# Kernel tuning notes

Measured on AMD Instinct MI355X. Metric: run time of the kernel, lower is better.

Reference implementation:

```python
import jax, jax.numpy as jnp
import numpy as np
from jax import lax

CW = 8       # current_window
PW = 8       # pretrain_window
HEADS = 8
LOG100 = float(np.log(100.0))


def setup_inputs() -> dict:
    key = jax.random.key(0)
    ks = jax.random.split(key, 8)
    B, H, W, C = 8, 126, 126, 256
    f32 = jnp.float32
    return {
        "x": jax.random.normal(ks[0], (B, H, W, C), f32),
        "w_qkv": jax.random.normal(ks[1], (C, 3 * C), f32) * 0.02,      # 1x1 conv, no bias
        "w_dw": jax.random.normal(ks[2], (3, 3, 1, 3 * C), f32) * 0.1,  # depthwise 3x3, HWIO
        "ln_gamma": jnp.ones((3 * C,), f32),
        "ln_beta": jnp.zeros((3 * C,), f32),
        "q_bias": jnp.zeros((C,), f32),
        "v_bias": jnp.zeros((C,), f32),
        "scale": jnp.full((HEADS, 1, 1), np.log(10.0), f32),
        "cpb_w0": jax.random.normal(ks[3], (2, 512), f32) * 0.02,
        "cpb_b0": jnp.zeros((512,), f32),
        "cpb_w1": jax.random.normal(ks[4], (512, HEADS), f32) * 0.02,   # no bias, sigmoid
        "w_proj": jax.random.normal(ks[5], (C, C), f32) * 0.02,
    }


def _l2n(t):
    # tf.math.l2_normalize with epsilon=1.55e-5
    return t * lax.rsqrt(jnp.maximum(jnp.sum(t * t, axis=-1, keepdims=True), 1.55e-5))


def _cpb_bias(cpb_w0, cpb_b0, cpb_w1, cw, L, heads):
    # log-spaced continuous relative position table (static)
    rel = np.arange(1 - cw, cw, dtype=np.float32)
    rel = np.stack(np.meshgrid(rel, rel, indexing='ij'), axis=-1)  # [2cw-1, 2cw-1, 2]
    rel = rel * (8.0 / (PW - 1.0))
    rel = np.sign(rel) * np.log1p(np.abs(rel)) / np.log(8.0)
    ri = np.arange(cw)
    ri = np.stack(np.meshgrid(ri, ri, indexing='ij'), axis=0).reshape(2, -1)
    ri = ri[:, :, None] - ri[:, None, :] + (cw - 1)
    relidx = (ri[0] * (2 * cw - 1) + ri[1]).reshape(-1)  # [L*L]
    h = jax.nn.relu(jnp.asarray(rel.reshape(-1, 2)) @ cpb_w0 + cpb_b0)
    bias = jax.nn.sigmoid(h @ cpb_w1) * 16.0             # [(2cw-1)^2, heads]
    bias = bias[jnp.asarray(relidx)].reshape(L, L, heads)
    return bias.transpose(2, 0, 1)                        # [heads, L, L]


def reference(x, w_qkv, w_dw, ln_gamma, ln_beta, q_bias, v_bias, scale,
              cpb_w0, cpb_b0, cpb_w1, w_proj):
    B, H, W, C = x.shape
    cw, heads = CW, HEADS
    hd = C // heads
    L = cw * cw

    # qkv 1x1 conv + depthwise 3x3 + layernorm (ConvNorm)
    qkv = jnp.einsum('bhwc,cd->bhwd', x, w_qkv)           # [B,H,W,3C]
    qkv = lax.conv_general_dilated(qkv, w_dw, (1, 1), 'SAME',
                                   dimension_numbers=('NHWC', 'HWIO', 'NHWC'),
                                   feature_group_count=3 * C)
    mu = jnp.mean(qkv, axis=-1, keepdims=True)
    var = jnp.mean(jnp.square(qkv - mu), axis=-1, keepdims=True)
    qkv = (qkv - mu) * lax.rsqrt(var + 1e-5) * ln_gamma + ln_beta
    qkv = qkv + jnp.concatenate([q_bias, jnp.zeros_like(q_bias), v_bias])

    # pad to multiple of window, grid-partition (MaxViT-style strided grid)
    pad_h, pad_w = (-H) % cw, (-W) % cw
    hb, wb = pad_h // 2, pad_w // 2
    qkv = jnp.pad(qkv, ((0, 0), (hb, pad_h - hb), (wb, pad_w - wb), (0, 0)))
    Hp, Wp = H + pad_h, W + pad_w
    Hb, Wb = Hp // cw, Wp // cw
    nw = Hb * Wb
    qkv = qkv.reshape(B, cw, Hb, cw, Wb, 3, heads, hd)
    qkv = qkv.transpose(0, 2, 4, 6, 1, 3, 5, 7).reshape(B * nw, heads, L, 3, hd)
    q, k, v = qkv[..., 0, :], qkv[..., 1, :], qkv[..., 2, :]

    # cosine attention with learned per-head log-scale (clamped at log 100)
    q, k = _l2n(q), _l2n(k)
    ls = jnp.exp(jnp.minimum(scale, LOG100))              # [heads,1,1]
    attn = jnp.einsum('nhqd,nhkd->nhqk', q * ls, k)

    attn = attn + _cpb_bias(cpb_w0, cpb_b0, cpb_w1, cw, L, heads)[None]

    if pad_h + pad_w > 0:
        m = jnp.pad(jnp.ones((1, H, W, 1), attn.dtype),
                    ((0, 0), (hb, pad_h - hb), (wb, pad_w - wb), (0, 0)))
        m = m.reshape(1, cw, Hb, cw, Wb, 1).transpose(0, 2, 4, 1, 3, 5).reshape(nw, L)
        mbias = -100.0 * (m == 0).astype(attn.dtype)       # [nw, L] over keys
        attn = attn.reshape(B, nw, heads, L, L) + mbias[None, :, None, None, :]
        attn = attn.reshape(B * nw, heads, L, L)

    attn = jax.nn.softmax(attn, axis=-1)
    out = jnp.einsum('nhqk,nhkd->nhqd', attn, v)           # [B*nw, heads, L, hd]

    # reverse grid partition + crop + projection
    out = out.reshape(B, Hb, Wb, heads, cw, cw, hd)
    out = out.transpose(0, 4, 1, 5, 2, 3, 6).reshape(B, Hp, Wp, C)
    out = out[:, hb:hb + H, wb:wb + W]
    return jnp.einsum('bhwc,cd->bhwd', out, w_proj)
```

## Files before the change

### kernel.cpp

```cpp
#include <hip/hip_runtime.h>

typedef unsigned short ushort;
typedef __bf16 bf16x8 __attribute__((ext_vector_type(8)));
typedef float f32x4 __attribute__((ext_vector_type(4)));
typedef float f4 __attribute__((ext_vector_type(4)));
typedef unsigned short us8 __attribute__((ext_vector_type(8)));
typedef unsigned short us4 __attribute__((ext_vector_type(4)));
typedef unsigned u32x4v __attribute__((ext_vector_type(4)));

#define NPIX 127008
#define HDIM 126
#define WDIM 126

__device__ __forceinline__ float bf2f(ushort u) {
  unsigned v = ((unsigned)u) << 16;
  return __builtin_bit_cast(float, v);
}
__device__ __forceinline__ ushort f2bf(float f) {
  unsigned x = __builtin_bit_cast(unsigned, f);
  x += 0x7fffu + ((x >> 16) & 1u);
  return (ushort)(x >> 16);
}

__global__ void k_cvt_x(const float* __restrict__ x, ushort* __restrict__ xb, int n8) {
  const int stride = gridDim.x * blockDim.x;
  for (int i = blockIdx.x * blockDim.x + threadIdx.x; i < n8; i += stride) {
    const f4 a = *(const f4*)&x[(size_t)i * 8];
    const f4 b = *(const f4*)&x[(size_t)i * 8 + 4];
    us8 o;
#pragma unroll
    for (int j = 0; j < 4; ++j) { o[j] = f2bf(a[j]); o[4 + j] = f2bf(b[j]); }
    *(us8*)&xb[(size_t)i * 8] = o;
  }
}

__global__ void k_cvt_wT(const float* __restrict__ in, ushort* __restrict__ out, int N, int K) {
  const int t = blockIdx.x * 256 + threadIdx.x;
  const int n = t / K, k = t - n * K;
  out[t] = f2bf(in[(size_t)k * N + n]);
}

__device__ __forceinline__ float frel(int i) {
  const float v = (float)(i - 7) * (8.0f / 7.0f);
  const float a = log1pf(fabsf(v)) * 0.4808983469629878f;
  return v < 0.f ? -a : a;
}

__global__ __launch_bounds__(256) void k_cpb1(const float* __restrict__ w0,
    const float* __restrict__ b0, const float* __restrict__ w1, float* __restrict__ tmp) {
  const int p = blockIdx.x * 4 + (threadIdx.x >> 6);
  const int lane = threadIdx.x & 63;
  if (p >= 225) return;
  const float r0 = frel(p / 15), r1 = frel(p % 15);
  float hv[8];
#pragma unroll
  for (int jj = 0; jj < 8; ++jj) {
    const int j = lane * 8 + jj;
    hv[jj] = fmaxf(0.f, r0 * w0[j] + r1 * w0[512 + j] + b0[j]);
  }
  for (int h = 0; h < 8; ++h) {
    float part = 0.f;
#pragma unroll
    for (int jj = 0; jj < 8; ++jj) part += hv[jj] * w1[(lane * 8 + jj) * 8 + h];
    for (int o = 32; o; o >>= 1) part += __shfl_xor(part, o);
    if (lane == 0) tmp[p * 8 + h] = 16.f / (1.f + __expf(-part));
  }
}

__global__ void k_cpb2(const float* __restrict__ tmp, float* __restrict__ biasV) {
  const int t = blockIdx.x * 256 + threadIdx.x;
  const int h = t >> 12, rest = t & 4095;
  const int ki = rest >> 10, g = (rest >> 8) & 3, q = (rest >> 2) & 63, r = rest & 3;
  const int key = ki * 16 + g * 4 + r;
  const int d0 = (q >> 3) - (key >> 3) + 7, d1 = (q & 7) - (key & 7) + 7;
  biasV[t] = tmp[(d0 * 15 + d1) * 8 + h];
}

#define GLL(g, l) __builtin_amdgcn_global_load_lds( \
    (const __attribute__((address_space(1))) void*)(g), \
    (__attribute__((address_space(3))) void*)(l), 16, 0, 0)

template <int OUTF, int NX>
__global__ __launch_bounds__(256) void k_gemm(const ushort* __restrict__ A,
                                              const ushort* __restrict__ Bt,
                                              void* __restrict__ Cv, int M, int N) {
  constexpr int K = 256;
  __shared__ ushort lsA[128 * 32];
  __shared__ ushort lsB[128 * 32];
  const int tid = threadIdx.x;
  const int wid = tid >> 6, lane = tid & 63;

  const int nwg = gridDim.x;
  const int q8 = nwg >> 3, r8 = nwg & 7;
  const int xcd = blockIdx.x & 7, pos = blockIdx.x >> 3;
  const int lin = (xcd < r8) ? xcd * (q8 + 1) + pos
                             : r8 * (q8 + 1) + (xcd - r8) * q8 + pos;
  const int m0 = (lin / NX) * 128, n0 = (lin % NX) * 128;

  f32x4 acc[4][4];
#pragma unroll
  for (int i = 0; i < 4; ++i)
#pragma unroll
    for (int j = 0; j < 4; ++j) acc[i][j] = 0.f;

  const int srow = tid >> 2, sk = (tid & 3) * 8;
  const int aw = (wid >> 1) * 64, bw = (wid & 1) * 64;
  const int fr = lane & 15, kg = (lane >> 4) * 8;
  char* lA = (char*)lsA + wid * 1024;
  char* lB = (char*)lsB + wid * 1024;

  int ra0 = m0 + srow;      if (ra0 >= M) ra0 = M - 1;
  int ra1 = m0 + srow + 64; if (ra1 >= M) ra1 = M - 1;
  const int rb0 = n0 + srow, rb1 = n0 + srow + 64;

  for (int kt = 0; kt < K; kt += 32) {
    __syncthreads();
    GLL(A + (size_t)ra0 * K + kt + sk, lA);
    GLL(A + (size_t)ra1 * K + kt + sk, lA + 4096);
    GLL(Bt + (size_t)rb0 * K + kt + sk, lB);
    GLL(Bt + (size_t)rb1 * K + kt + sk, lB + 4096);
    __syncthreads();
    bf16x8 af[4], bb[4];
#pragma unroll
    for (int i = 0; i < 4; ++i)
      af[i] = *(const bf16x8*)&lsA[(aw + i * 16 + fr) * 32 + kg];
#pragma unroll
    for (int j = 0; j < 4; ++j)
      bb[j] = *(const bf16x8*)&lsB[(bw + j * 16 + fr) * 32 + kg];
#pragma unroll
    for (int i = 0; i < 4; ++i)
#pragma unroll
      for (int j = 0; j < 4; ++j)
        acc[i][j] = __builtin_amdgcn_mfma_f32_16x16x32_bf16(af[i], bb[j], acc[i][j], 0, 0, 0);
  }

  const int r4 = (lane >> 4) * 4, cc = lane & 15;
#pragma unroll
  for (int i = 0; i < 4; ++i) {
#pragma unroll
    for (int j = 0; j < 4; ++j) {
      const int gc = n0 + bw + j * 16 + cc;
#pragma unroll
      for (int r = 0; r < 4; ++r) {
        const int gr = m0 + aw + i * 16 + r4 + r;
        if (gr < M) {
          if constexpr (OUTF == 0)
            ((ushort*)Cv)[(size_t)gr * N + gc] = f2bf(acc[i][j][r]);
          else
            ((float*)Cv)[(size_t)gr * N + gc] = acc[i][j][r];
        }
      }
    }
  }
}

__global__ __launch_bounds__(192) void k_convln(const ushort* __restrict__ pre,
    const float* __restrict__ wdw,
    const float* __restrict__ gamma, const float* __restrict__ beta,
    const float* __restrict__ qb, const float* __restrict__ vb,
    const float* __restrict__ scale, ushort* __restrict__ qkvw) {
  __shared__ __align__(16) float red[2][3][4];
  const int nwg = gridDim.x;
  const int q8 = nwg >> 3, r8 = nwg & 7;
  const int xcd = blockIdx.x & 7, pos = blockIdx.x >> 3;
  const int lin = (xcd < r8) ? xcd * (q8 + 1) + pos
                             : r8 * (q8 + 1) + (xcd - r8) * q8 + pos;
  const int rowid = lin % 1008;
  const int seg = lin / 1008;
  const int b = rowid / HDIM, h = rowid - b * HDIM;
  const int chunk = threadIdx.x;
  const int wid = chunk >> 6, lane = chunk & 63;
  const int c0 = chunk * 4;

  float wt[9][4];
#pragma unroll
  for (int tap = 0; tap < 9; ++tap) {
    const f4 wa = *(const f4*)&wdw[tap * 768 + c0];
#pragma unroll
    for (int j = 0; j < 4; ++j) wt[tap][j] = wa[j];
  }
  if (h == 0) {
#pragma unroll
    for (int tap = 0; tap < 3; ++tap)
#pragma unroll
      for (int j = 0; j < 4; ++j) wt[tap][j] = 0.f;
  }
  if (h == HDIM - 1) {
#pragma unroll
    for (int tap = 6; tap < 9; ++tap)
#pragma unroll
      for (int j = 0; j < 4; ++j) wt[tap][j] = 0.f;
  }

  const f4 g4 = *(const f4*)&gamma[c0];
  const f4 b4 = *(const f4*)&beta[c0];
  f4 addb = {0.f, 0.f, 0.f, 0.f};
  if (wid == 0) addb = *(const f4*)&qb[c0];
  if (wid == 2) addb = *(const f4*)&vb[c0 - 512];
  const float ls = (wid == 0) ? __expf(fminf(scale[chunk >> 3], 4.60517025f)) : 1.f;

  const int hm = h > 0 ? h - 1 : 0, hp2 = h < HDIM - 1 ? h + 1 : HDIM - 1;
  const ushort* r0 = pre + (size_t)((b * HDIM + hm) * WDIM) * 768 + c0;
  const ushort* r1 = pre + (size_t)((b * HDIM + h) * WDIM) * 768 + c0;
  const ushort* r2 = pre + (size_t)((b * HDIM + hp2) * WDIM) * 768 + c0;

  const int w0 = seg * 6;
  float n0[3][4], n1[3][4], n2[3][4], n3[3][4], n4[3][4], n5[3][4];

#define LOADCOL(dst, w)                                                   \
  {                                                                       \
    us4 u0 = *(const us4*)&r0[(size_t)(w) * 768];                         \
    us4 u1 = *(const us4*)&r1[(size_t)(w) * 768];                         \
    us4 u2 = *(const us4*)&r2[(size_t)(w) * 768];                         \
    _Pragma("unroll") for (int j = 0; j < 4; ++j) {                       \
      dst[0][j] = bf2f(u0[j]); dst[1][j] = bf2f(u1[j]); dst[2][j] = bf2f(u2[j]); } \
  }
#define ZEROCOL(dst)                                                      \
  { _Pragma("unroll") for (int rr = 0; rr < 3; ++rr)                      \
    _Pragma("unroll") for (int j = 0; j < 4; ++j) dst[rr][j] = 0.f; }

  if (w0 > 0) { LOADCOL(n0, w0 - 1) } else { ZEROCOL(n0) }
  LOADCOL(n1, w0)
  LOADCOL(n2, w0 + 1)
  LOADCOL(n3, w0 + 2)

  const int dstc = ((b << 8) + (((h + 1) & 15) << 4)) << 6;
  const int dsth = ((h + 1) >> 4) << 3;

#define EPI(acc, tS, tQ, wp_)                                             \
  {                                                                       \
    const float mu = (tS) * (1.f / 768.f);                                \
    const float var = (tQ) * (1.f / 768.f) - mu * mu;                     \
    const float rs = rsqrtf(var + 1e-5f);                                 \
    float y[4];                                                           \
    _Pragma("unroll") for (int j = 0; j < 4; ++j)                         \
      y[j] = (acc[j] - mu) * rs * g4[j] + b4[j] + addb[j];                \
    if (wid < 2) {                                                        \
      float gg = y[0]*y[0] + y[1]*y[1] + y[2]*y[2] + y[3]*y[3];           \
      gg += __shfl_xor(gg, 1); gg += __shfl_xor(gg, 2); gg += __shfl_xor(gg, 4); \
      const float rn = rsqrtf(fmaxf(gg, 1.55e-5f)) * ls;                  \
      _Pragma("unroll") for (int j = 0; j < 4; ++j) y[j] *= rn;           \
    }                                                                     \
    const int dstrow = dstc + (((wp_) & 15) << 6) + dsth + ((wp_) >> 4);  \
    us4 o;                                                                \
    _Pragma("unroll") for (int j = 0; j < 4; ++j) o[j] = f2bf(y[j]);      \
    *(us4*)&qkvw[(size_t)dstrow * 768 + c0] = o;                          \
  }

#define CORE(A, B, C, D, w)                                               \
    float a0[4], a1[4];                                                   \
    _Pragma("unroll") for (int j = 0; j < 4; ++j) {                       \
      a0[j] = A[0][j]*wt[0][j] + B[0][j]*wt[1][j] + C[0][j]*wt[2][j]      \
            + A[1][j]*wt[3][j] + B[1][j]*wt[4][j] + C[1][j]*wt[5][j]      \
            + A[2][j]*wt[6][j] + B[2][j]*wt[7][j] + C[2][j]*wt[8][j];     \
      a1[j] = B[0][j]*wt[0][j] + C[0][j]*wt[1][j] + D[0][j]*wt[2][j]      \
            + B[1][j]*wt[3][j] + C[1][j]*wt[4][j] + D[1][j]*wt[5][j]      \
            + B[2][j]*wt[6][j] + C[2][j]*wt[7][j] + D[2][j]*wt[8][j];     \
    }                                                                     \
    float s0 = a0[0]+a0[1]+a0[2]+a0[3];                                   \
    float p0 = a0[0]*a0[0]+a0[1]*a0[1]+a0[2]*a0[2]+a0[3]*a0[3];           \
    float s1 = a1[0]+a1[1]+a1[2]+a1[3];                                   \
    float p1 = a1[0]*a1[0]+a1[1]*a1[1]+a1[2]*a1[2]+a1[3]*a1[3];           \
    _Pragma("unroll") for (int o = 32; o; o >>= 1) {                      \
      s0 += __shfl_xor(s0, o); p0 += __shfl_xor(p0, o);                   \
      s1 += __shfl_xor(s1, o); p1 += __shfl_xor(p1, o); }                 \
    const int par = ((w) >> 1) & 1;                                       \
    if (lane == 0) { f4 rv = {s0, p0, s1, p1}; *(f4*)&red[par][wid][0] = rv; } \
    asm volatile("s_waitcnt lgkmcnt(0)" ::: "memory");                    \
    __builtin_amdgcn_s_barrier();                                         \
    asm volatile("" ::: "memory");                                        \
    const float t0 = red[par][0][0] + red[par][1][0] + red[par][2][0];    \
    const float u0_ = red[par][0][1] + red[par][1][1] + red[par][2][1];   \
    const float t1 = red[par][0][2] + red[par][1][2] + red[par][2][2];    \
    const float u1_ = red[par][0][3] + red[par][1][3] + red[par][2][3];   \
    EPI(a0, t0, u0_, (w) + 1)                                             \
    EPI(a1, t1, u1_, (w) + 2)

#define PHASE(A, B, C, D, E, F, w)                                        \
  {                                                                       \
    if ((w) + 3 < WDIM) { LOADCOL(E, (w) + 3) } else { ZEROCOL(E) }       \
    if ((w) + 4 < WDIM) { LOADCOL(F, (w) + 4) } else { ZEROCOL(F) }       \
    CORE(A, B, C, D, w)                                                   \
  }
#define PHASE_LAST(A, B, C, D, w)                                         \
  {                                                                       \
    CORE(A, B, C, D, w)                                                   \
  }

  PHASE(n0, n1, n2, n3, n4, n5, w0)
  PHASE(n2, n3, n4, n5, n0, n1, w0 + 2)
  PHASE_LAST(n4, n5, n0, n1, w0 + 4)
#undef PHASE
#undef PHASE_LAST
#undef CORE
#undef EPI
#undef LOADCOL
#undef ZEROCOL
}

__global__ __launch_bounds__(256) void k_attn(const ushort* __restrict__ qkvw,
    const float* __restrict__ biasV, ushort* __restrict__ aout) {
  __shared__ ushort Vs[4][64][36];
  const int wid = threadIdx.x >> 6, lane = threadIdx.x & 63;
  const int u = blockIdx.x * 4 + wid;
  const int head = u >> 11, wl = u & 2047;
  const int b = wl >> 8, wh = (wl >> 4) & 15, ww = wl & 15;
  const int c = lane & 15, g = lane >> 4;
  const int g4 = g * 4, g8 = g * 8;
  const ushort* wb = qkvw + (size_t)wl * 64 * 768;
  const us8 zz = 0;

  const bool e_r0 = (wh == 0), e_r7 = (wh == 15), e_c0 = (ww == 0), e_c7 = (ww == 15);
#define TOKVALID(t) (!(((e_r0) & (((t) >> 3) == 0)) | ((e_r7) & (((t) >> 3) == 7)) | \
                       ((e_c0) & (((t) & 7) == 0)) | ((e_c7) & (((t) & 7) == 7))))

  {
    const bool tv = TOKVALID(lane);
    const ushort* vp = wb + (size_t)lane * 768 + 512 + head * 32;
    us8 v0 = *(const us8*)vp;
    us8 v1 = *(const us8*)(vp + 8);
    us8 v2 = *(const us8*)(vp + 16);
    us8 v3 = *(const us8*)(vp + 24);
    v0 = tv ? v0 : zz;
    v1 = tv ? v1 : zz;
    v2 = tv ? v2 : zz;
    v3 = tv ? v3 : zz;
    ushort* vr = &Vs[wid][lane][0];
    *(us4*)&vr[0]  = __builtin_shufflevector(v0, v0, 0, 1, 2, 3);
    *(us4*)&vr[4]  = __builtin_shufflevector(v0, v0, 4, 5, 6, 7);
    *(us4*)&vr[8]  = __builtin_shufflevector(v1, v1, 0, 1, 2, 3);
    *(us4*)&vr[12] = __builtin_shufflevector(v1, v1, 4, 5, 6, 7);
    *(us4*)&vr[16] = __builtin_shufflevector(v2, v2, 0, 1, 2, 3);
    *(us4*)&vr[20] = __builtin_shufflevector(v2, v2, 4, 5, 6, 7);
    *(us4*)&vr[24] = __builtin_shufflevector(v3, v3, 0, 1, 2, 3);
    *(us4*)&vr[28] = __builtin_shufflevector(v3, v3, 4, 5, 6, 7);
  }

  bf16x8 kf[4], qf[4];
#pragma unroll
  for (int ki = 0; ki < 4; ++ki) {
    const int tk = ki * 16 + c;
    us8 kv = *(const us8*)&wb[(size_t)tk * 768 + 256 + head * 32 + g8];
    kv = TOKVALID(tk) ? kv : zz;
    kf[ki] = __builtin_bit_cast(bf16x8, kv);
  }
#pragma unroll
  for (int qj = 0; qj < 4; ++qj) {
    const int tq = qj * 16 + c;
    us8 qv = *(const us8*)&wb[(size_t)tq * 768 + head * 32 + g8];
    qv = TOKVALID(tq) ? qv : zz;
    qf[qj] = __builtin_bit_cast(bf16x8, qv);
  }

  const float* bvh = biasV + (head << 12);
  f32x4 st[4][4];
#pragma unroll
  for (int ki = 0; ki < 4; ++ki)
#pragma unroll
    for (int qj = 0; qj < 4; ++qj) {
      const f32x4 bfrag = *(const f32x4*)&bvh[((ki * 4 + g) << 8) + ((qj * 16 + c) << 2)];
      st[ki][qj] = __builtin_amdgcn_mfma_f32_16x16x32_bf16(kf[ki], qf[qj], bfrag, 0, 0, 0);
    }

  unsigned afr[4][2][4];
#pragma unroll
  for (int qj = 0; qj < 4; ++qj) {
    float s[16];
#pragma unroll
    for (int ki = 0; ki < 4; ++ki)
#pragma unroll
      for (int r = 0; r < 4; ++r) {
        const int key = ki * 16 + g4 + r;
        s[ki * 4 + r] = TOKVALID(key) ? st[ki][qj][r] : -1e30f;
      }
    float m = s[0];
#pragma unroll
    for (int i = 1; i < 16; ++i) m = fmaxf(m, s[i]);
    m = fmaxf(m, __shfl_xor(m, 16));
    m = fmaxf(m, __shfl_xor(m, 32));
    float den = 0.f;
#pragma unroll
    for (int i = 0; i < 16; ++i) { s[i] = __expf(s[i] - m); den += s[i]; }
    den += __shfl_xor(den, 16);
    den += __shfl_xor(den, 32);
    const float inv = 1.f / den;

    unsigned pk[4][2];
#pragma unroll
    for (int ki = 0; ki < 4; ++ki) {
      pk[ki][0] = ((unsigned)f2bf(s[ki * 4 + 1] * inv) << 16) | f2bf(s[ki * 4 + 0] * inv);
      pk[ki][1] = ((unsigned)f2bf(s[ki * 4 + 3] * inv) << 16) | f2bf(s[ki * 4 + 2] * inv);
    }
#pragma unroll
    for (int j2 = 0; j2 < 4; ++j2) {
      const int src = c + 16 * (2 * (g & 1) + (j2 >> 1));
      const unsigned s0 = __shfl(pk[0][j2 & 1], src);
      const unsigned s1 = __shfl(pk[1][j2 & 1], src);
      const unsigned s2 = __shfl(pk[2][j2 & 1], src);
      const unsigned s3 = __shfl(pk[3][j2 & 1], src);
      afr[qj][0][j2] = (g < 2) ? s0 : s1;
      afr[qj][1][j2] = (g < 2) ? s2 : s3;
    }
  }

  f32x4 ao[4][2];
#pragma unroll
  for (int qi = 0; qi < 4; ++qi)
#pragma unroll
    for (int di = 0; di < 2; ++di) ao[qi][di] = 0.f;
#pragma unroll
  for (int kc = 0; kc < 2; ++kc) {
#pragma unroll
    for (int di = 0; di < 2; ++di) {
      us8 bv;
#pragma unroll
      for (int j = 0; j < 8; ++j) bv[j] = Vs[wid][kc * 32 + g8 + j][di * 16 + c];
      const bf16x8 bb = __builtin_bit_cast(bf16x8, bv);
#pragma unroll
      for (int qi = 0; qi < 4; ++qi) {
        const u32x4v aw4 = {afr[qi][kc][0], afr[qi][kc][1], afr[qi][kc][2], afr[qi][kc][3]};
        ao[qi][di] = __builtin_amdgcn_mfma_f32_16x16x32_bf16(
            __builtin_bit_cast(bf16x8, aw4), bb, ao[qi][di], 0, 0, 0);
      }
    }
  }

#pragma unroll
  for (int qi = 0; qi < 4; ++qi)
#pragma unroll
    for (int r = 0; r < 4; ++r) {
      const int q = qi * 16 + g4 + r;
      if (TOKVALID(q)) {
        const int h = (q >> 3) * 16 + wh - 1, w2 = (q & 7) * 16 + ww - 1;
        ushort* op = aout + ((size_t)((b * HDIM + h) * WDIM + w2)) * 256 + head * 32;
        op[c] = f2bf(ao[qi][0][r]);
        op[16 + c] = f2bf(ao[qi][1][r]);
      }
    }
#undef TOKVALID
}

extern "C" void kernel_launch(void* const* d_in, const int* in_sizes, int n_in,
                              void* d_out, int out_size, void* d_ws, size_t ws_size,
                              hipStream_t stream) {
  (void)in_sizes; (void)n_in; (void)out_size; (void)ws_size;
  const float* x      = (const float*)d_in[0];
  const float* w_qkv  = (const float*)d_in[1];
  const float* w_dw   = (const float*)d_in[2];
  const float* ln_g   = (const float*)d_in[3];
  const float* ln_b   = (const float*)d_in[4];
  const float* q_bias = (const float*)d_in[5];
  const float* v_bias = (const float*)d_in[6];
  const float* scale  = (const float*)d_in[7];
  const float* cpb_w0 = (const float*)d_in[8];
  const float* cpb_b0 = (const float*)d_in[9];
  const float* cpb_w1 = (const float*)d_in[10];
  const float* w_proj = (const float*)d_in[11];
  float* out = (float*)d_out;

  char* ws = (char*)d_ws;
  const size_t PRE  = (size_t)NPIX * 768 * 2;
  const size_t QKVW = (size_t)131072 * 768 * 2;
  ushort* pre    = (ushort*)ws;
  ushort* qkvw   = (ushort*)(ws + PRE);
  ushort* xb     = (ushort*)(ws + PRE);
  ushort* aoutb  = pre;
  ushort* wqkvT  = (ushort*)(ws + PRE + QKVW);
  ushort* wprojT = (ushort*)(ws + PRE + QKVW + (size_t)768 * 256 * 2);
  float*  cpbtmp = (float*)(ws + PRE + QKVW + (size_t)768 * 256 * 2 + (size_t)256 * 256 * 2);
  float*  biasV  = (float*)(ws + PRE + QKVW + (size_t)768 * 256 * 2 + (size_t)256 * 256 * 2 + 8192);

  k_cvt_wT<<<768, 256, 0, stream>>>(w_qkv, wqkvT, 768, 256);
  k_cvt_wT<<<256, 256, 0, stream>>>(w_proj, wprojT, 256, 256);
  k_cpb1<<<57, 256, 0, stream>>>(cpb_w0, cpb_b0, cpb_w1, cpbtmp);
  k_cpb2<<<128, 256, 0, stream>>>(cpbtmp, biasV);
  k_cvt_x<<<2048, 256, 0, stream>>>(x, xb, NPIX * 256 / 8);
  k_gemm<0, 6><<<5958, 256, 0, stream>>>(xb, wqkvT, pre, NPIX, 768);
  k_convln<<<21168, 192, 0, stream>>>(pre, w_dw, ln_g, ln_b, q_bias, v_bias, scale, qkvw);
  k_attn<<<4096, 256, 0, stream>>>(qkvw, biasV, aoutb);
  k_gemm<1, 2><<<1986, 256, 0, stream>>>(aoutb, wprojT, out, NPIX, 256);
}
```

Measured before the change: 479.3 us.

## Double GEMM K-tile to 64 and remap attention blocks for XCD locality

The GEMM K-step goes from 32 to 64, which halves the number of barrier pairs per tile and issues 8 MFMAs per operand load batch. LDS use per block doubles. The attention kernel remaps block indices so the heads of the same window are adjacent and blocks are spread across XCDs, so each XCD's L2 is reused for the shared qkv window data. The larger LDS footprint may lower occupancy.

```diff
diff --git a/kernel.cpp b/kernel.cpp
--- a/kernel.cpp
+++ b/kernel.cpp
@@ -85,8 +85,8 @@
                                               const ushort* __restrict__ Bt,
                                               void* __restrict__ Cv, int M, int N) {
   constexpr int K = 256;
-  __shared__ ushort lsA[128 * 32];
-  __shared__ ushort lsB[128 * 32];
+  __shared__ ushort lsA[128 * 64];
+  __shared__ ushort lsB[128 * 64];
   const int tid = threadIdx.x;
   const int wid = tid >> 6, lane = tid & 63;
 
@@ -103,35 +103,43 @@
 #pragma unroll
     for (int j = 0; j < 4; ++j) acc[i][j] = 0.f;
 
-  const int srow = tid >> 2, sk = (tid & 3) * 8;
+  const int srow = tid >> 3, sk = (tid & 7) * 8;
   const int aw = (wid >> 1) * 64, bw = (wid & 1) * 64;
   const int fr = lane & 15, kg = (lane >> 4) * 8;
   char* lA = (char*)lsA + wid * 1024;
   char* lB = (char*)lsB + wid * 1024;
 
-  int ra0 = m0 + srow;      if (ra0 >= M) ra0 = M - 1;
-  int ra1 = m0 + srow + 64; if (ra1 >= M) ra1 = M - 1;
-  const int rb0 = n0 + srow, rb1 = n0 + srow + 64;
-
-  for (int kt = 0; kt < K; kt += 32) {
+  int ra[4];
+#pragma unroll
+  for (int c = 0; c < 4; ++c) {
+    int r = m0 + c * 32 + srow;
+    ra[c] = r < M ? r : M - 1;
+  }
+  const int rb0 = n0 + srow;
+
+  for (int kt = 0; kt < K; kt += 64) {
     __syncthreads();
-    GLL(A + (size_t)ra0 * K + kt + sk, lA);
-    GLL(A + (size_t)ra1 * K + kt + sk, lA + 4096);
-    GLL(Bt + (size_t)rb0 * K + kt + sk, lB);
-    GLL(Bt + (size_t)rb1 * K + kt + sk, lB + 4096);
+#pragma unroll
+    for (int c = 0; c < 4; ++c) {
+      GLL(A + (size_t)ra[c] * K + kt + sk, lA + c * 4096);
+      GLL(Bt + (size_t)(rb0 + c * 32) * K + kt + sk, lB + c * 4096);
+    }
     __syncthreads();
-    bf16x8 af[4], bb[4];
-#pragma unroll
-    for (int i = 0; i < 4; ++i)
-      af[i] = *(const bf16x8*)&lsA[(aw + i * 16 + fr) * 32 + kg];
-#pragma unroll
-    for (int j = 0; j < 4; ++j)
-      bb[j] = *(const bf16x8*)&lsB[(bw + j * 16 + fr) * 32 + kg];
-#pragma unroll
-    for (int i = 0; i < 4; ++i)
-#pragma unroll
-      for (int j = 0; j < 4; ++j)
-        acc[i][j] = __builtin_amdgcn_mfma_f32_16x16x32_bf16(af[i], bb[j], acc[i][j], 0, 0, 0);
+    bf16x8 af[2][4], bb[2][4];
+#pragma unroll
+    for (int kk = 0; kk < 2; ++kk)
+#pragma unroll
+      for (int i = 0; i < 4; ++i) {
+        af[kk][i] = *(const bf16x8*)&lsA[(aw + i * 16 + fr) * 64 + kk * 32 + kg];
+        bb[kk][i] = *(const bf16x8*)&lsB[(bw + i * 16 + fr) * 64 + kk * 32 + kg];
+      }
+#pragma unroll
+    for (int kk = 0; kk < 2; ++kk)
+#pragma unroll
+      for (int i = 0; i < 4; ++i)
+#pragma unroll
+        for (int j = 0; j < 4; ++j)
+          acc[i][j] = __builtin_amdgcn_mfma_f32_16x16x32_bf16(af[kk][i], bb[kk][j], acc[i][j], 0, 0, 0);
   }
 
   const int r4 = (lane >> 4) * 4, cc = lane & 15;
@@ -302,8 +310,9 @@
     const float* __restrict__ biasV, ushort* __restrict__ aout) {
   __shared__ ushort Vs[4][64][36];
   const int wid = threadIdx.x >> 6, lane = threadIdx.x & 63;
-  const int u = blockIdx.x * 4 + wid;
-  const int head = u >> 11, wl = u & 2047;
+  const int linb = (blockIdx.x & 7) * 512 + (blockIdx.x >> 3);
+  const int u = linb * 4 + wid;
+  const int head = u & 7, wl = u >> 3;
   const int b = wl >> 8, wh = (wl >> 4) & 15, ww = wl & 15;
   const int c = lane & 15, g = lane >> 4;
   const int g4 = g * 4, g8 = g * 8;
```

Measured after the change: 461.3 us. -3.7%, faster.
